# Performance work log

Hardware: AMD Instinct MI355X
Metric: run time of the kernel (lower is better)

## Reference

```python
import jax, jax.numpy as jnp
import numpy as np

IM_SIZE = (256, 256)
OVERSAMP = 1.25
WIDTH = 6
BETA = float(np.pi * np.sqrt((WIDTH / OVERSAMP * (OVERSAMP - 0.5)) ** 2 - 0.8))
OS_SIZE = tuple(int(np.ceil(OVERSAMP * n)) for n in IM_SIZE)  # (320, 320)
D = 2


def _kb(x):
    # Kaiser-Bessel interpolation kernel: i0(beta*sqrt(1-x^2)) for |x|<=1 (sigpy convention)
    return jnp.i0(BETA * jnp.sqrt(jnp.maximum(1.0 - x * x, 0.0)))


def setup_inputs() -> dict:
    key = jax.random.key(0)
    k1, k2, k3 = jax.random.split(key, 3)
    N, C = 1, 8
    img_r = jax.random.normal(k1, (N, C) + IM_SIZE, dtype=jnp.float32)
    img_i = jax.random.normal(k2, (N, C) + IM_SIZE, dtype=jnp.float32)
    # trajectory in [-N_i/2, N_i/2] per the class docstring
    trj = (jax.random.uniform(k3, (N, 64, 4096, D), dtype=jnp.float32) - 0.5) * 256.0
    return {"img_r": img_r, "img_i": img_i, "trj": trj}


def _nufft_forward(img_r, img_i, trj):
    img = (img_r + 1j * img_i).astype(jnp.complex64)  # (N, C, H, W)
    nd = img.ndim
    # --- apodization (inverse FT of KB kernel), separable per axis ---
    for a in range(D):
        n, osn = IM_SIZE[a], OS_SIZE[a]
        idx = jnp.arange(n, dtype=jnp.float32)
        arg = jnp.sqrt(BETA ** 2 - (np.pi * WIDTH * (idx - n // 2) / osn) ** 2)
        apod = arg / jnp.sinh(arg)
        shape = [1] * nd
        shape[nd - D + a] = n
        img = img * apod.reshape(shape)
    # --- scale + centered zero-pad to oversampled grid ---
    img = img / np.sqrt(float(np.prod(IM_SIZE)))
    pads = [(0, 0)] * (nd - D) + [(((o - n) // 2), (o - n) - ((o - n) // 2))
                                  for n, o in zip(IM_SIZE, OS_SIZE)]
    img = jnp.pad(img, pads)
    # --- centered FFT (ifftshift -> fftn(norm=None) -> fftshift) ---
    axes = tuple(range(-D, 0))
    ksp_os = jnp.fft.fftshift(jnp.fft.fftn(jnp.fft.ifftshift(img, axes=axes), axes=axes), axes=axes)
    # --- scale trajectory to oversampled grid coordinates ---
    scale = jnp.array([OS_SIZE[a] / IM_SIZE[a] for a in range(D)], jnp.float32)
    shift = jnp.array([OS_SIZE[a] // 2 for a in range(D)], jnp.float32)
    coord = trj * scale + shift  # (N, R, S, 2)
    x0 = jnp.ceil(coord - WIDTH / 2.0)
    # --- KB interpolation: fixed 6x6 neighbor loop, vectorized gather over all points ---
    N = img.shape[0]
    out = jnp.zeros((N,) + img.shape[1:nd - D] + coord.shape[1:-1], jnp.complex64)

    def gather(grid, ix, iy):  # grid (C, Hos, Wos), ix/iy (R, S) -> (C, R, S)
        return grid[:, ix, iy]

    for dx in range(WIDTH):
        px = x0[..., 0] + dx
        wx = _kb((px - coord[..., 0]) / (WIDTH / 2.0))
        ix = px.astype(jnp.int32) % OS_SIZE[0]
        for dy in range(WIDTH):
            py = x0[..., 1] + dy
            wy = _kb((py - coord[..., 1]) / (WIDTH / 2.0))
            iy = py.astype(jnp.int32) % OS_SIZE[1]
            vals = jax.vmap(gather)(ksp_os, ix, iy)  # (N, C, R, S)
            out = out + vals * (wx * wy)[:, None, :, :]
    return out / (WIDTH ** D)


def reference(img_r, img_i, trj):
    return _nufft_forward(img_r, img_i, trj)
```

## Files before the change

### kernel.cpp

```cpp
#include <hip/hip_runtime.h>
#include <math.h>

#define NCH   8
#define IMN   256
#define OSN   320
#define NPTS  (64*4096)
#define KD    512
#define BETA_F   10.9551078f
#define BETA2_F  120.014389f
#define APOD_C   0.05890486225f

typedef unsigned short u16;
typedef unsigned int   u32;
typedef __attribute__((ext_vector_type(8))) short s16x8;
typedef __attribute__((ext_vector_type(4))) float f32x4;

__device__ __forceinline__ u32 f2bf(float f) {
    u32 u = __float_as_uint(f);
    return (u + 0x7FFFu + ((u >> 16) & 1u)) >> 16;
}

__device__ __forceinline__ float i0f(float t) {
    if (t < 3.75f) {
        float y = t * t * (1.0f / 14.0625f);
        return 1.0f + y * (3.5156229f + y * (3.0899424f + y * (1.2067492f +
                     y * (0.2659732f + y * (0.0360768f + y * 0.0045813f)))));
    }
    float z = 3.75f / t;
    float p = 0.39894228f + z * (0.01328592f + z * (0.00225319f + z * (-0.00157565f +
              z * (0.00916281f + z * (-0.02057706f + z * (0.02635537f +
              z * (-0.01647633f + z * 0.00392377f)))))));
    return expf(t) * rsqrtf(t) * p;
}

__device__ __forceinline__ float apodf(int i) {
    float x = APOD_C * (float)(i - IMN / 2);
    float arg = sqrtf(BETA2_F - x * x);
    float e = expf(arg);
    float sh = 0.5f * (e - 1.0f / e);
    return arg / sh;
}

__global__ void prep_const(u32* __restrict__ B1, u32* __restrict__ B2) {
    int idx = blockIdx.x * 256 + threadIdx.x;
    int k = idx >> 8, j = idx & 255;
    int p = (k * (j + 32)) % OSN;
    float th = (2.0f * (float)M_PI / (float)OSN) * (float)p;
    float s = ((k + j) & 1) ? -1.0f : 1.0f;
    float sn, cs;
    sincosf(th, &sn, &cs);
    float re = s * cs, im = -s * sn;
    B1[idx] = f2bf(re) | (f2bf(-im) << 16);
    B2[idx] = f2bf(im) | (f2bf(re) << 16);
}

__global__ void prep_a(const float* __restrict__ r, const float* __restrict__ im,
                       u32* __restrict__ A) {
    int idx = blockIdx.x * 256 + threadIdx.x;
    int i2 = idx & 255, i1 = (idx >> 8) & 255;
    float w = apodf(i1) * apodf(i2) * (1.0f / 256.0f);
    A[idx] = f2bf(r[idx] * w) | (f2bf(im[idx] * w) << 16);
}

__launch_bounds__(128)
__global__ void gemm1(const short* __restrict__ Abf, const short* __restrict__ B1,
                      const short* __restrict__ B2, short* __restrict__ Tb) {
    const int c = blockIdx.z;
    const int mBase = blockIdx.y * 64;
    const int nBase = blockIdx.x * 32;
    __shared__ short As[64][40], B1s[32][40], B2s[32][40];
    const int t = threadIdx.x;
    const int l = t & 63, w = t >> 6;
    const int arow = t >> 1, aseg = (t & 1) * 16;
    const int brow = t >> 2, bseg = (t & 3) * 8;
    const int fm = l & 15, fq = (l >> 4) * 8;
    f32x4 zz = {0.f, 0.f, 0.f, 0.f};
    f32x4 accRe[2][2], accIm[2][2];
    #pragma unroll
    for (int i = 0; i < 2; i++)
        #pragma unroll
        for (int j = 0; j < 2; j++) { accRe[i][j] = zz; accIm[i][j] = zz; }

    for (int kc = 0; kc < 16; kc++) {
        const int kb = kc * 32;
        {
            const short* ap = Abf + ((long)(c * IMN + mBase + arow)) * KD + kb + aseg;
            *(s16x8*)&As[arow][aseg]     = *(const s16x8*)(ap);
            *(s16x8*)&As[arow][aseg + 8] = *(const s16x8*)(ap + 8);
        }
        *(s16x8*)&B1s[brow][bseg] = *(const s16x8*)(B1 + (long)(nBase + brow) * KD + kb + bseg);
        *(s16x8*)&B2s[brow][bseg] = *(const s16x8*)(B2 + (long)(nBase + brow) * KD + kb + bseg);
        __syncthreads();
        s16x8 a0  = *(const s16x8*)&As [w * 32 + fm][fq];
        s16x8 a1  = *(const s16x8*)&As [w * 32 + 16 + fm][fq];
        s16x8 b10 = *(const s16x8*)&B1s[fm][fq];
        s16x8 b11 = *(const s16x8*)&B1s[16 + fm][fq];
        s16x8 b20 = *(const s16x8*)&B2s[fm][fq];
        s16x8 b21 = *(const s16x8*)&B2s[16 + fm][fq];
        accRe[0][0] = __builtin_amdgcn_mfma_f32_16x16x32_bf16(a0, b10, accRe[0][0], 0, 0, 0);
        accRe[0][1] = __builtin_amdgcn_mfma_f32_16x16x32_bf16(a0, b11, accRe[0][1], 0, 0, 0);
        accRe[1][0] = __builtin_amdgcn_mfma_f32_16x16x32_bf16(a1, b10, accRe[1][0], 0, 0, 0);
        accRe[1][1] = __builtin_amdgcn_mfma_f32_16x16x32_bf16(a1, b11, accRe[1][1], 0, 0, 0);
        accIm[0][0] = __builtin_amdgcn_mfma_f32_16x16x32_bf16(a0, b20, accIm[0][0], 0, 0, 0);
        accIm[0][1] = __builtin_amdgcn_mfma_f32_16x16x32_bf16(a0, b21, accIm[0][1], 0, 0, 0);
        accIm[1][0] = __builtin_amdgcn_mfma_f32_16x16x32_bf16(a1, b20, accIm[1][0], 0, 0, 0);
        accIm[1][1] = __builtin_amdgcn_mfma_f32_16x16x32_bf16(a1, b21, accIm[1][1], 0, 0, 0);
        __syncthreads();
    }
    #pragma unroll
    for (int i = 0; i < 2; i++)
        #pragma unroll
        for (int j = 0; j < 2; j++) {
            int i1b = mBase + w * 32 + i * 16 + (l >> 4) * 4;
            int k2  = nBase + j * 16 + fm;
            s16x8 v;
            #pragma unroll
            for (int r = 0; r < 4; r++) {
                v[2 * r]     = (short)f2bf(accRe[i][j][r]);
                v[2 * r + 1] = (short)f2bf(accIm[i][j][r]);
            }
            *(s16x8*)(Tb + ((long)(c * OSN + k2)) * KD + 2 * i1b) = v;
        }
}

__launch_bounds__(128)
__global__ void gemm2(const short* __restrict__ B1, const short* __restrict__ B2,
                      const short* __restrict__ Tb, u32* __restrict__ Gb) {
    const int c = blockIdx.z;
    const int mBase = blockIdx.y * 64;
    const int nBase = blockIdx.x * 32;
    __shared__ short A1s[64][40], A2s[64][40], Bs[32][40];
    const int t = threadIdx.x;
    const int l = t & 63, w = t >> 6;
    const int arow = t >> 1, aseg = (t & 1) * 16;
    const int brow = t >> 2, bseg = (t & 3) * 8;
    const int fm = l & 15, fq = (l >> 4) * 8;
    f32x4 zz = {0.f, 0.f, 0.f, 0.f};
    f32x4 accRe[2][2], accIm[2][2];
    #pragma unroll
    for (int i = 0; i < 2; i++)
        #pragma unroll
        for (int j = 0; j < 2; j++) { accRe[i][j] = zz; accIm[i][j] = zz; }

    for (int kc = 0; kc < 16; kc++) {
        const int kb = kc * 32;
        {
            const short* a1p = B1 + (long)(mBase + arow) * KD + kb + aseg;
            const short* a2p = B2 + (long)(mBase + arow) * KD + kb + aseg;
            *(s16x8*)&A1s[arow][aseg]     = *(const s16x8*)(a1p);
            *(s16x8*)&A1s[arow][aseg + 8] = *(const s16x8*)(a1p + 8);
            *(s16x8*)&A2s[arow][aseg]     = *(const s16x8*)(a2p);
            *(s16x8*)&A2s[arow][aseg + 8] = *(const s16x8*)(a2p + 8);
        }
        *(s16x8*)&Bs[brow][bseg] = *(const s16x8*)(Tb + ((long)(c * OSN + nBase + brow)) * KD + kb + bseg);
        __syncthreads();
        s16x8 a10 = *(const s16x8*)&A1s[w * 32 + fm][fq];
        s16x8 a11 = *(const s16x8*)&A1s[w * 32 + 16 + fm][fq];
        s16x8 a20 = *(const s16x8*)&A2s[w * 32 + fm][fq];
        s16x8 a21 = *(const s16x8*)&A2s[w * 32 + 16 + fm][fq];
        s16x8 b0  = *(const s16x8*)&Bs [fm][fq];
        s16x8 b1  = *(const s16x8*)&Bs [16 + fm][fq];
        accRe[0][0] = __builtin_amdgcn_mfma_f32_16x16x32_bf16(a10, b0, accRe[0][0], 0, 0, 0);
        accRe[0][1] = __builtin_amdgcn_mfma_f32_16x16x32_bf16(a10, b1, accRe[0][1], 0, 0, 0);
        accRe[1][0] = __builtin_amdgcn_mfma_f32_16x16x32_bf16(a11, b0, accRe[1][0], 0, 0, 0);
        accRe[1][1] = __builtin_amdgcn_mfma_f32_16x16x32_bf16(a11, b1, accRe[1][1], 0, 0, 0);
        accIm[0][0] = __builtin_amdgcn_mfma_f32_16x16x32_bf16(a20, b0, accIm[0][0], 0, 0, 0);
        accIm[0][1] = __builtin_amdgcn_mfma_f32_16x16x32_bf16(a20, b1, accIm[0][1], 0, 0, 0);
        accIm[1][0] = __builtin_amdgcn_mfma_f32_16x16x32_bf16(a21, b0, accIm[1][0], 0, 0, 0);
        accIm[1][1] = __builtin_amdgcn_mfma_f32_16x16x32_bf16(a21, b1, accIm[1][1], 0, 0, 0);
        __syncthreads();
    }
    #pragma unroll
    for (int i = 0; i < 2; i++)
        #pragma unroll
        for (int j = 0; j < 2; j++) {
            int k2 = nBase + j * 16 + fm;
            #pragma unroll
            for (int r = 0; r < 4; r++) {
                int k1 = mBase + w * 32 + i * 16 + (l >> 4) * 4 + r;
                Gb[((long)k1 * OSN + k2) * NCH + c] =
                    f2bf(accRe[i][j][r]) | (f2bf(accIm[i][j][r]) << 16);
            }
        }
}

__global__ void interp_kernel(const float* __restrict__ trj,
                              const u32* __restrict__ grid,
                              u32* __restrict__ out) {
    const int t = threadIdx.x;
    const int pl = t >> 2;
    const int cp = (t & 3) * 2;
    __shared__ float wxs[64][6], wys[64][6];
    __shared__ int   x0s[64], y0s[64];

    if (t < 64) {
        int pt = blockIdx.x * 64 + t;
        float2 tv = *(const float2*)(trj + pt * 2);
        float cx = __fadd_rn(__fmul_rn(tv.x, 1.25f), 160.0f);
        float cy = __fadd_rn(__fmul_rn(tv.y, 1.25f), 160.0f);
        float x0 = ceilf(__fadd_rn(cx, -3.0f));
        float y0 = ceilf(__fadd_rn(cy, -3.0f));
        x0s[t] = (int)x0;
        y0s[t] = (int)y0;
        #pragma unroll
        for (int d = 0; d < 6; d++) {
            float u = __fdiv_rn(__fsub_rn(x0 + (float)d, cx), 3.0f);
            wxs[t][d] = i0f(BETA_F * sqrtf(fmaxf(1.0f - u * u, 0.0f)));
            float ww = __fdiv_rn(__fsub_rn(y0 + (float)d, cy), 3.0f);
            wys[t][d] = i0f(BETA_F * sqrtf(fmaxf(1.0f - ww * ww, 0.0f)));
        }
    }
    __syncthreads();

    int ix[6], iy[6];
    const int x0i = x0s[pl], y0i = y0s[pl];
    #pragma unroll
    for (int d = 0; d < 6; d++) {
        int vx = x0i + d;
        ix[d] = ((vx % OSN) + OSN) % OSN;
        int vy = y0i + d;
        iy[d] = ((vy % OSN) + OSN) % OSN;
    }

    float re0 = 0.f, im0 = 0.f, re1 = 0.f, im1 = 0.f;
    #pragma unroll
    for (int dx = 0; dx < 6; dx++) {
        long base = (long)ix[dx] * OSN;
        float wxv = wxs[pl][dx];
        #pragma unroll
        for (int dy = 0; dy < 6; dy++) {
            uint2 g = *(const uint2*)(grid + (base + iy[dy]) * NCH + cp);
            float ww = wxv * wys[pl][dy];
            re0 += __uint_as_float(g.x << 16) * ww;
            im0 += __uint_as_float(g.x & 0xFFFF0000u) * ww;
            re1 += __uint_as_float(g.y << 16) * ww;
            im1 += __uint_as_float(g.y & 0xFFFF0000u) * ww;
        }
    }
    re0 *= (1.0f / 36.0f); im0 *= (1.0f / 36.0f);
    re1 *= (1.0f / 36.0f); im1 *= (1.0f / 36.0f);

    __shared__ float2 lds[64 * 8];
    lds[pl * 8 + cp]     = make_float2(re0, im0);
    lds[pl * 8 + cp + 1] = make_float2(re1, im1);
    __syncthreads();
    int c2 = t >> 5, p2 = t & 31;
    float2 va = lds[p2 * 8 + c2];
    float2 vb = lds[(p2 + 32) * 8 + c2];
    long ob = (long)c2 * NPTS + blockIdx.x * 64;
    out[ob + p2]      = f2bf(va.y) | (f2bf(va.x) << 16);
    out[ob + p2 + 32] = f2bf(vb.y) | (f2bf(vb.x) << 16);
}

extern "C" void kernel_launch(void* const* d_in, const int* in_sizes, int n_in,
                              void* d_out, int out_size, void* d_ws, size_t ws_size,
                              hipStream_t stream) {
    const float* img_r = (const float*)d_in[0];
    const float* img_i = (const float*)d_in[1];
    const float* trj   = (const float*)d_in[2];

    char* ob = (char*)d_out;
    short* Tb  = (short*)(ob);
    u32*  B1u  = (u32*)(ob + 2621440);
    u32*  B2u  = (u32*)(ob + 2949120);
    u32*  Au   = (u32*)(ob + 3276800);
    u32*  Gb   = (u32*)d_ws;

    prep_const<<<(OSN * IMN) / 256, 256, 0, stream>>>(B1u, B2u);
    prep_a<<<(NCH * IMN * IMN) / 256, 256, 0, stream>>>(img_r, img_i, Au);
    gemm1<<<dim3(OSN / 32, IMN / 64, NCH), 128, 0, stream>>>(
        (const short*)Au, (const short*)B1u, (const short*)B2u, Tb);
    gemm2<<<dim3(OSN / 32, OSN / 64, NCH), 128, 0, stream>>>(
        (const short*)B1u, (const short*)B2u, Tb, Gb);
    interp_kernel<<<NPTS / 64, 256, 0, stream>>>(trj, Gb, (u32*)d_out);
}
```

Before: 116.9 us.

## Merge prep kernels, single-wave double-buffered GEMMs, spread interp weight computation across threads

Merges the two prep kernels into one launch that branches on block index. Both DFT GEMM kernels become single-wavefront 32x32-tile blocks. They register-prefetch the next K chunk into double-buffered LDS and drop __syncthreads, since a single wave needs no block barrier. The interpolation kernel now spreads the 12 per-point KB weight evaluations over all 256 threads instead of 64. This cuts launch overhead, barrier stalls and serial weight work, but halves the GEMM tile height and so adds blocks and redundant B-matrix loads.

```diff
diff --git a/kernel.cpp b/kernel.cpp
--- a/kernel.cpp
+++ b/kernel.cpp
@@ -41,39 +41,42 @@
     return arg / sh;
 }
 
-__global__ void prep_const(u32* __restrict__ B1, u32* __restrict__ B2) {
-    int idx = blockIdx.x * 256 + threadIdx.x;
-    int k = idx >> 8, j = idx & 255;
-    int p = (k * (j + 32)) % OSN;
-    float th = (2.0f * (float)M_PI / (float)OSN) * (float)p;
-    float s = ((k + j) & 1) ? -1.0f : 1.0f;
-    float sn, cs;
-    sincosf(th, &sn, &cs);
-    float re = s * cs, im = -s * sn;
-    B1[idx] = f2bf(re) | (f2bf(-im) << 16);
-    B2[idx] = f2bf(im) | (f2bf(re) << 16);
-}
-
-__global__ void prep_a(const float* __restrict__ r, const float* __restrict__ im,
-                       u32* __restrict__ A) {
-    int idx = blockIdx.x * 256 + threadIdx.x;
-    int i2 = idx & 255, i1 = (idx >> 8) & 255;
-    float w = apodf(i1) * apodf(i2) * (1.0f / 256.0f);
-    A[idx] = f2bf(r[idx] * w) | (f2bf(im[idx] * w) << 16);
-}
-
-__launch_bounds__(128)
+__global__ void prep(const float* __restrict__ r, const float* __restrict__ im,
+                     u32* __restrict__ B1, u32* __restrict__ B2,
+                     u32* __restrict__ A) {
+    const int b = blockIdx.x, t = threadIdx.x;
+    if (b < (OSN * IMN) / 256) {
+        int idx = b * 256 + t;
+        int k = idx >> 8, j = idx & 255;
+        int p = (k * (j + 32)) % OSN;
+        float th = (2.0f * (float)M_PI / (float)OSN) * (float)p;
+        float s = ((k + j) & 1) ? -1.0f : 1.0f;
+        float sn, cs;
+        sincosf(th, &sn, &cs);
+        float re = s * cs, imv = -s * sn;
+        B1[idx] = f2bf(re) | (f2bf(-imv) << 16);
+        B2[idx] = f2bf(imv) | (f2bf(re) << 16);
+    } else {
+        int idx = (b - (OSN * IMN) / 256) * 256 + t;
+        int i2 = idx & 255, i1 = (idx >> 8) & 255;
+        float w = apodf(i1) * apodf(i2) * (1.0f / 256.0f);
+        A[idx] = f2bf(r[idx] * w) | (f2bf(im[idx] * w) << 16);
+    }
+}
+
+__launch_bounds__(64)
 __global__ void gemm1(const short* __restrict__ Abf, const short* __restrict__ B1,
                       const short* __restrict__ B2, short* __restrict__ Tb) {
     const int c = blockIdx.z;
-    const int mBase = blockIdx.y * 64;
+    const int mBase = blockIdx.y * 32;
     const int nBase = blockIdx.x * 32;
-    __shared__ short As[64][40], B1s[32][40], B2s[32][40];
+    __shared__ short As[2][32][36], B1s[2][32][36], B2s[2][32][36];
     const int t = threadIdx.x;
-    const int l = t & 63, w = t >> 6;
-    const int arow = t >> 1, aseg = (t & 1) * 16;
-    const int brow = t >> 2, bseg = (t & 3) * 8;
-    const int fm = l & 15, fq = (l >> 4) * 8;
+    const int row = t >> 1, seg = (t & 1) * 16;
+    const int fm = t & 15, fq = (t >> 4) * 8;
+    const short* ap  = Abf + (long)(c * IMN + mBase + row) * KD + seg;
+    const short* b1p = B1 + (long)(nBase + row) * KD + seg;
+    const short* b2p = B2 + (long)(nBase + row) * KD + seg;
     f32x4 zz = {0.f, 0.f, 0.f, 0.f};
     f32x4 accRe[2][2], accIm[2][2];
     #pragma unroll
@@ -81,22 +84,37 @@
         #pragma unroll
         for (int j = 0; j < 2; j++) { accRe[i][j] = zz; accIm[i][j] = zz; }
 
+    s16x8 c0 = *(const s16x8*)(ap);
+    s16x8 c1 = *(const s16x8*)(ap + 8);
+    s16x8 c2 = *(const s16x8*)(b1p);
+    s16x8 c3 = *(const s16x8*)(b1p + 8);
+    s16x8 c4 = *(const s16x8*)(b2p);
+    s16x8 c5 = *(const s16x8*)(b2p + 8);
+
+    #pragma unroll
     for (int kc = 0; kc < 16; kc++) {
-        const int kb = kc * 32;
-        {
-            const short* ap = Abf + ((long)(c * IMN + mBase + arow)) * KD + kb + aseg;
-            *(s16x8*)&As[arow][aseg]     = *(const s16x8*)(ap);
-            *(s16x8*)&As[arow][aseg + 8] = *(const s16x8*)(ap + 8);
-        }
-        *(s16x8*)&B1s[brow][bseg] = *(const s16x8*)(B1 + (long)(nBase + brow) * KD + kb + bseg);
-        *(s16x8*)&B2s[brow][bseg] = *(const s16x8*)(B2 + (long)(nBase + brow) * KD + kb + bseg);
-        __syncthreads();
-        s16x8 a0  = *(const s16x8*)&As [w * 32 + fm][fq];
-        s16x8 a1  = *(const s16x8*)&As [w * 32 + 16 + fm][fq];
-        s16x8 b10 = *(const s16x8*)&B1s[fm][fq];
-        s16x8 b11 = *(const s16x8*)&B1s[16 + fm][fq];
-        s16x8 b20 = *(const s16x8*)&B2s[fm][fq];
-        s16x8 b21 = *(const s16x8*)&B2s[16 + fm][fq];
+        const int buf = kc & 1;
+        *(s16x8*)&As [buf][row][seg]     = c0;
+        *(s16x8*)&As [buf][row][seg + 8] = c1;
+        *(s16x8*)&B1s[buf][row][seg]     = c2;
+        *(s16x8*)&B1s[buf][row][seg + 8] = c3;
+        *(s16x8*)&B2s[buf][row][seg]     = c4;
+        *(s16x8*)&B2s[buf][row][seg + 8] = c5;
+        if (kc < 15) {
+            const int kb = (kc + 1) * 32;
+            c0 = *(const s16x8*)(ap + kb);
+            c1 = *(const s16x8*)(ap + kb + 8);
+            c2 = *(const s16x8*)(b1p + kb);
+            c3 = *(const s16x8*)(b1p + kb + 8);
+            c4 = *(const s16x8*)(b2p + kb);
+            c5 = *(const s16x8*)(b2p + kb + 8);
+        }
+        s16x8 a0  = *(const s16x8*)&As [buf][fm][fq];
+        s16x8 a1  = *(const s16x8*)&As [buf][16 + fm][fq];
+        s16x8 b10 = *(const s16x8*)&B1s[buf][fm][fq];
+        s16x8 b11 = *(const s16x8*)&B1s[buf][16 + fm][fq];
+        s16x8 b20 = *(const s16x8*)&B2s[buf][fm][fq];
+        s16x8 b21 = *(const s16x8*)&B2s[buf][16 + fm][fq];
         accRe[0][0] = __builtin_amdgcn_mfma_f32_16x16x32_bf16(a0, b10, accRe[0][0], 0, 0, 0);
         accRe[0][1] = __builtin_amdgcn_mfma_f32_16x16x32_bf16(a0, b11, accRe[0][1], 0, 0, 0);
         accRe[1][0] = __builtin_amdgcn_mfma_f32_16x16x32_bf16(a1, b10, accRe[1][0], 0, 0, 0);
@@ -105,13 +123,12 @@
         accIm[0][1] = __builtin_amdgcn_mfma_f32_16x16x32_bf16(a0, b21, accIm[0][1], 0, 0, 0);
         accIm[1][0] = __builtin_amdgcn_mfma_f32_16x16x32_bf16(a1, b20, accIm[1][0], 0, 0, 0);
         accIm[1][1] = __builtin_amdgcn_mfma_f32_16x16x32_bf16(a1, b21, accIm[1][1], 0, 0, 0);
-        __syncthreads();
     }
     #pragma unroll
     for (int i = 0; i < 2; i++)
         #pragma unroll
         for (int j = 0; j < 2; j++) {
-            int i1b = mBase + w * 32 + i * 16 + (l >> 4) * 4;
+            int i1b = mBase + i * 16 + (t >> 4) * 4;
             int k2  = nBase + j * 16 + fm;
             s16x8 v;
             #pragma unroll
@@ -123,18 +140,19 @@
         }
 }
 
-__launch_bounds__(128)
+__launch_bounds__(64)
 __global__ void gemm2(const short* __restrict__ B1, const short* __restrict__ B2,
                       const short* __restrict__ Tb, u32* __restrict__ Gb) {
     const int c = blockIdx.z;
-    const int mBase = blockIdx.y * 64;
+    const int mBase = blockIdx.y * 32;
     const int nBase = blockIdx.x * 32;
-    __shared__ short A1s[64][40], A2s[64][40], Bs[32][40];
+    __shared__ short A1s[2][32][36], A2s[2][32][36], Bs[2][32][36];
     const int t = threadIdx.x;
-    const int l = t & 63, w = t >> 6;
-    const int arow = t >> 1, aseg = (t & 1) * 16;
-    const int brow = t >> 2, bseg = (t & 3) * 8;
-    const int fm = l & 15, fq = (l >> 4) * 8;
+    const int row = t >> 1, seg = (t & 1) * 16;
+    const int fm = t & 15, fq = (t >> 4) * 8;
+    const short* a1p = B1 + (long)(mBase + row) * KD + seg;
+    const short* a2p = B2 + (long)(mBase + row) * KD + seg;
+    const short* bp  = Tb + ((long)(c * OSN + nBase + row)) * KD + seg;
     f32x4 zz = {0.f, 0.f, 0.f, 0.f};
     f32x4 accRe[2][2], accIm[2][2];
     #pragma unroll
@@ -142,24 +160,37 @@
         #pragma unroll
         for (int j = 0; j < 2; j++) { accRe[i][j] = zz; accIm[i][j] = zz; }
 
+    s16x8 c0 = *(const s16x8*)(a1p);
+    s16x8 c1 = *(const s16x8*)(a1p + 8);
+    s16x8 c2 = *(const s16x8*)(a2p);
+    s16x8 c3 = *(const s16x8*)(a2p + 8);
+    s16x8 c4 = *(const s16x8*)(bp);
+    s16x8 c5 = *(const s16x8*)(bp + 8);
+
+    #pragma unroll
     for (int kc = 0; kc < 16; kc++) {
-        const int kb = kc * 32;
-        {
-            const short* a1p = B1 + (long)(mBase + arow) * KD + kb + aseg;
-            const short* a2p = B2 + (long)(mBase + arow) * KD + kb + aseg;
-            *(s16x8*)&A1s[arow][aseg]     = *(const s16x8*)(a1p);
-            *(s16x8*)&A1s[arow][aseg + 8] = *(const s16x8*)(a1p + 8);
-            *(s16x8*)&A2s[arow][aseg]     = *(const s16x8*)(a2p);
-            *(s16x8*)&A2s[arow][aseg + 8] = *(const s16x8*)(a2p + 8);
-        }
-        *(s16x8*)&Bs[brow][bseg] = *(const s16x8*)(Tb + ((long)(c * OSN + nBase + brow)) * KD + kb + bseg);
-        __syncthreads();
-        s16x8 a10 = *(const s16x8*)&A1s[w * 32 + fm][fq];
-        s16x8 a11 = *(const s16x8*)&A1s[w * 32 + 16 + fm][fq];
-        s16x8 a20 = *(const s16x8*)&A2s[w * 32 + fm][fq];
-        s16x8 a21 = *(const s16x8*)&A2s[w * 32 + 16 + fm][fq];
-        s16x8 b0  = *(const s16x8*)&Bs [fm][fq];
-        s16x8 b1  = *(const s16x8*)&Bs [16 + fm][fq];
+        const int buf = kc & 1;
+        *(s16x8*)&A1s[buf][row][seg]     = c0;
+        *(s16x8*)&A1s[buf][row][seg + 8] = c1;
+        *(s16x8*)&A2s[buf][row][seg]     = c2;
+        *(s16x8*)&A2s[buf][row][seg + 8] = c3;
+        *(s16x8*)&Bs [buf][row][seg]     = c4;
+        *(s16x8*)&Bs [buf][row][seg + 8] = c5;
+        if (kc < 15) {
+            const int kb = (kc + 1) * 32;
+            c0 = *(const s16x8*)(a1p + kb);
+            c1 = *(const s16x8*)(a1p + kb + 8);
+            c2 = *(const s16x8*)(a2p + kb);
+            c3 = *(const s16x8*)(a2p + kb + 8);
+            c4 = *(const s16x8*)(bp + kb);
+            c5 = *(const s16x8*)(bp + kb + 8);
+        }
+        s16x8 a10 = *(const s16x8*)&A1s[buf][fm][fq];
+        s16x8 a11 = *(const s16x8*)&A1s[buf][16 + fm][fq];
+        s16x8 a20 = *(const s16x8*)&A2s[buf][fm][fq];
+        s16x8 a21 = *(const s16x8*)&A2s[buf][16 + fm][fq];
+        s16x8 b0  = *(const s16x8*)&Bs [buf][fm][fq];
+        s16x8 b1  = *(const s16x8*)&Bs [buf][16 + fm][fq];
         accRe[0][0] = __builtin_amdgcn_mfma_f32_16x16x32_bf16(a10, b0, accRe[0][0], 0, 0, 0);
         accRe[0][1] = __builtin_amdgcn_mfma_f32_16x16x32_bf16(a10, b1, accRe[0][1], 0, 0, 0);
         accRe[1][0] = __builtin_amdgcn_mfma_f32_16x16x32_bf16(a11, b0, accRe[1][0], 0, 0, 0);
@@ -168,7 +199,6 @@
         accIm[0][1] = __builtin_amdgcn_mfma_f32_16x16x32_bf16(a20, b1, accIm[0][1], 0, 0, 0);
         accIm[1][0] = __builtin_amdgcn_mfma_f32_16x16x32_bf16(a21, b0, accIm[1][0], 0, 0, 0);
         accIm[1][1] = __builtin_amdgcn_mfma_f32_16x16x32_bf16(a21, b1, accIm[1][1], 0, 0, 0);
-        __syncthreads();
     }
     #pragma unroll
     for (int i = 0; i < 2; i++)
@@ -177,7 +207,7 @@
             int k2 = nBase + j * 16 + fm;
             #pragma unroll
             for (int r = 0; r < 4; r++) {
-                int k1 = mBase + w * 32 + i * 16 + (l >> 4) * 4 + r;
+                int k1 = mBase + i * 16 + (t >> 4) * 4 + r;
                 Gb[((long)k1 * OSN + k2) * NCH + c] =
                     f2bf(accRe[i][j][r]) | (f2bf(accIm[i][j][r]) << 16);
             }
@@ -193,22 +223,23 @@
     __shared__ float wxs[64][6], wys[64][6];
     __shared__ int   x0s[64], y0s[64];
 
-    if (t < 64) {
-        int pt = blockIdx.x * 64 + t;
-        float2 tv = *(const float2*)(trj + pt * 2);
-        float cx = __fadd_rn(__fmul_rn(tv.x, 1.25f), 160.0f);
-        float cy = __fadd_rn(__fmul_rn(tv.y, 1.25f), 160.0f);
-        float x0 = ceilf(__fadd_rn(cx, -3.0f));
-        float y0 = ceilf(__fadd_rn(cy, -3.0f));
-        x0s[t] = (int)x0;
-        y0s[t] = (int)y0;
-        #pragma unroll
-        for (int d = 0; d < 6; d++) {
-            float u = __fdiv_rn(__fsub_rn(x0 + (float)d, cx), 3.0f);
-            wxs[t][d] = i0f(BETA_F * sqrtf(fmaxf(1.0f - u * u, 0.0f)));
-            float ww = __fdiv_rn(__fsub_rn(y0 + (float)d, cy), 3.0f);
-            wys[t][d] = i0f(BETA_F * sqrtf(fmaxf(1.0f - ww * ww, 0.0f)));
-        }
+    #pragma unroll
+    for (int k = 0; k < 3; k++) {
+        int e = t + 256 * k;
+        int ptl = e / 12;
+        int rem = e - ptl * 12;
+        int axis = rem >= 6 ? 1 : 0;
+        int d = rem - axis * 6;
+        int pt = blockIdx.x * 64 + ptl;
+        float tv = trj[pt * 2 + axis];
+        float cc = __fadd_rn(__fmul_rn(tv, 1.25f), 160.0f);
+        float v0 = ceilf(__fadd_rn(cc, -3.0f));
+        if (d == 0) {
+            if (axis) y0s[ptl] = (int)v0; else x0s[ptl] = (int)v0;
+        }
+        float u = __fdiv_rn(__fsub_rn(v0 + (float)d, cc), 3.0f);
+        float wv = i0f(BETA_F * sqrtf(fmaxf(1.0f - u * u, 0.0f)));
+        if (axis) wys[ptl][d] = wv; else wxs[ptl][d] = wv;
     }
     __syncthreads();
 
@@ -266,11 +297,11 @@
     u32*  Au   = (u32*)(ob + 3276800);
     u32*  Gb   = (u32*)d_ws;
 
-    prep_const<<<(OSN * IMN) / 256, 256, 0, stream>>>(B1u, B2u);
-    prep_a<<<(NCH * IMN * IMN) / 256, 256, 0, stream>>>(img_r, img_i, Au);
-    gemm1<<<dim3(OSN / 32, IMN / 64, NCH), 128, 0, stream>>>(
+    prep<<<(OSN * IMN) / 256 + (NCH * IMN * IMN) / 256, 256, 0, stream>>>(
+        img_r, img_i, B1u, B2u, Au);
+    gemm1<<<dim3(OSN / 32, IMN / 32, NCH), 64, 0, stream>>>(
         (const short*)Au, (const short*)B1u, (const short*)B2u, Tb);
-    gemm2<<<dim3(OSN / 32, OSN / 64, NCH), 128, 0, stream>>>(
+    gemm2<<<dim3(OSN / 32, OSN / 32, NCH), 64, 0, stream>>>(
         (const short*)B1u, (const short*)B2u, Tb, Gb);
     interp_kernel<<<NPTS / 64, 256, 0, stream>>>(trj, Gb, (u32*)d_out);
 }
```

After: 111.9 us. 1.04x faster.
